# Kernel optimization log

Measured on AMD Instinct MI355X. Metric: run time of the kernel, lower is better.

The kernel has to match this reference:

```python
import jax, jax.numpy as jnp
import numpy as np

N = 50000      # nodes
E = 800000     # edges (avg degree 16)
NF, EF, H, OUT, K = 16, 8, 64, 8, 3
N_MID = 2      # n_gnn_layers=4 -> first + 2 mid + last


def setup_inputs() -> dict:
    key = jax.random.key(0)
    ks = jax.random.split(key, 16)
    s = 0.05
    return {
        "x": jax.random.normal(ks[0], (N, NF), dtype=jnp.float32),
        "edge_index": jax.random.randint(ks[1], (2, E), 0, N, dtype=jnp.int64),
        "edge_attr": jax.random.normal(ks[2], (E, EF), dtype=jnp.float32),
        # edge_aggr MLP: Linear(EF,H) -> ReLU -> Linear(H,1)
        "mlp_W1": jax.random.normal(ks[3], (EF, H), dtype=jnp.float32) * s,
        "mlp_b1": jnp.zeros((H,), dtype=jnp.float32),
        "mlp_W2": jax.random.normal(ks[4], (H, 1), dtype=jnp.float32) * s,
        "mlp_b2": jnp.zeros((1,), dtype=jnp.float32),
        # TAGConv-style layers: K+1 linear maps each
        "W_first": jax.random.normal(ks[5], (K + 1, NF, H), dtype=jnp.float32) * s,
        "b_first": jnp.zeros((H,), dtype=jnp.float32),
        "W_mid": jax.random.normal(ks[6], (N_MID, K + 1, H, H), dtype=jnp.float32) * s,
        "b_mid": jnp.zeros((N_MID, H), dtype=jnp.float32),
        "W_last": jax.random.normal(ks[7], (K + 1, H, OUT), dtype=jnp.float32) * s,
        "b_last": jnp.zeros((OUT,), dtype=jnp.float32),
    }


def _gcn_norm(edge_weight, src, dst, n_nodes):
    # deg computed at target (col), D^{-1/2} A D^{-1/2}, no self loops
    deg = jax.ops.segment_sum(edge_weight, dst, num_segments=n_nodes)
    dinv = jnp.where(deg > 0, jax.lax.rsqrt(jnp.where(deg > 0, deg, 1.0)), 0.0)
    return dinv[src] * edge_weight * dinv[dst]  # [E]


def _tag_conv(x, Ws, b, src, dst, norm, n_nodes):
    # out = sum_k (A_norm^k x) W_k + b
    out = x @ Ws[0]
    h = x
    for k in range(1, Ws.shape[0]):
        h = jax.ops.segment_sum(h[src] * norm[:, None], dst, num_segments=n_nodes)
        out = out + h @ Ws[k]
    return out + b


def reference(x, edge_index, edge_attr, mlp_W1, mlp_b1, mlp_W2, mlp_b2,
              W_first, b_first, W_mid, b_mid, W_last, b_last):
    src, dst = edge_index[0], edge_index[1]
    n_nodes = x.shape[0]
    # edge MLP -> scalar edge weight per edge
    ew = (jax.nn.relu(edge_attr @ mlp_W1 + mlp_b1) @ mlp_W2 + mlp_b2)[:, 0]  # [E]
    norm = _gcn_norm(ew, src, dst, n_nodes)
    h = jax.nn.relu(_tag_conv(x, W_first, b_first, src, dst, norm, n_nodes))
    for i in range(W_mid.shape[0]):
        h = jax.nn.relu(_tag_conv(h, W_mid[i], b_mid[i], src, dst, norm, n_nodes))
    return _tag_conv(h, W_last, b_last, src, dst, norm, n_nodes)
```

## Files before the change

### kernel.cpp

```cpp
#include <hip/hip_runtime.h>
#include <stdint.h>

#define N_NODES 50000
#define N_EDGES 800000
#define NFEAT   16
#define EFEAT   8
#define HID     64
#define OUTF    8
#define NMID    2
#define NX      (N_NODES * NFEAT)
#define NPW     16
#define CAP     64
#define PGB     ((N_NODES + 4 * NPW - 1) / (4 * NPW))
#define PPB     ((N_NODES + 15) / 16)
#define NWB     ((N_NODES + 3) / 4)

typedef unsigned short ushort_t;
typedef unsigned int   uint_t;
typedef unsigned long long ull_t;
typedef __bf16 bf16x8 __attribute__((ext_vector_type(8)));
typedef float  f32x4  __attribute__((ext_vector_type(4)));

__device__ __forceinline__ float b2f(ushort_t u) {
    return __uint_as_float(((uint_t)u) << 16);
}
__device__ __forceinline__ ushort_t f2b(float f) {
    uint_t u = __float_as_uint(f);
    return (ushort_t)((u + 0x7fffu + ((u >> 16) & 1u)) >> 16);
}
__device__ __forceinline__ float h2f(ushort_t u) {
    union { ushort_t u; _Float16 h; } c; c.u = u; return (float)c.h;
}
__device__ __forceinline__ ushort_t f2h(float f) {
    union { ushort_t u; _Float16 h; } c; c.h = (_Float16)f; return c.u;
}

__global__ __launch_bounds__(256) void edge_mlp_kernel(
    const float* __restrict__ ea, const float* __restrict__ x,
    const int* __restrict__ ei,
    const float* __restrict__ W1, const float* __restrict__ b1,
    const float* __restrict__ W2, const float* __restrict__ b2,
    ushort_t* __restrict__ xb, float* __restrict__ ew,
    int* __restrict__ cnts, uint_t* __restrict__ bucket)
{
    int tid = threadIdx.x;
    int e = blockIdx.x * 256 + tid;
    if (e >= N_EDGES) return;

    int d = ei[N_EDGES + e];
    int pos = atomicAdd(&cnts[d], 1);
    if (pos < CAP)
        bucket[(size_t)d * CAP + pos] = (uint_t)e;

    xb[e] = f2b(x[e]);

    float4 v0 = ((const float4*)ea)[2 * e];
    float4 v1 = ((const float4*)ea)[2 * e + 1];
    float a[8] = {v0.x, v0.y, v0.z, v0.w, v1.x, v1.y, v1.z, v1.w};

    float h[HID];
    #pragma unroll
    for (int j = 0; j < HID; ++j) h[j] = b1[j];

    #pragma unroll
    for (int i = 0; i < EFEAT; ++i) {
        float ai = a[i];
        #pragma unroll
        for (int j = 0; j < HID; ++j)
            h[j] = fmaf(ai, W1[i * HID + j], h[j]);
    }

    float acc = b2[0];
    #pragma unroll
    for (int j = 0; j < HID; ++j)
        acc = fmaf(fmaxf(h[j], 0.f), W2[j], acc);

    ew[e] = acc;
}

__global__ __launch_bounds__(256) void degdinv_kernel(
    int* __restrict__ cnts, const uint_t* __restrict__ bucket,
    const float* __restrict__ ew, float* __restrict__ dinv)
{
    int tid = threadIdx.x;
    int n = blockIdx.x * 4 + (tid >> 6);
    int lane = tid & 63;
    if (n >= N_NODES) return;
    int c = cnts[n]; if (c > CAP) c = CAP;
    float w = 0.f;
    if (lane < c)
        w = ew[bucket[(size_t)n * CAP + lane]];
    #pragma unroll
    for (int o = 32; o; o >>= 1) w += __shfl_down(w, o, 64);
    if (lane == 0) {
        cnts[n] = c;
        dinv[n] = (w > 0.f) ? (1.f / sqrtf(w)) : 0.f;
    }
}

__global__ __launch_bounds__(256) void rescale_kernel(
    const int* __restrict__ cnts, const float* __restrict__ dinv,
    const float* __restrict__ ew, const int* __restrict__ ei,
    uint_t* __restrict__ bucket)
{
    int tid = threadIdx.x;
    int n = blockIdx.x * 4 + (tid >> 6);
    int lane = tid & 63;
    if (n >= N_NODES) return;
    int c = cnts[n];
    float dn = dinv[n];
    if (lane < c) {
        uint_t e = bucket[(size_t)n * CAP + lane];
        int s = ei[e];
        float nv = dinv[s] * ew[e] * dn;
        nv = fminf(fmaxf(nv, -60000.f), 60000.f);
        bucket[(size_t)n * CAP + lane] = (((uint_t)f2h(nv)) << 16) | (uint_t)s;
    }
}

template<int W>
__global__ __launch_bounds__(256, 6) void prop_kernel(
    const ushort_t* __restrict__ gsrc, ushort_t* __restrict__ gout,
    const int* __restrict__ cnts, const uint_t* __restrict__ bucket)
{
    int tid = threadIdx.x;
    int wv = tid >> 6, lane = tid & 63;
    int nb = (blockIdx.x * 4 + wv) * 4;
    if (nb >= N_NODES) return;

    int cv = (lane < 4) ? cnts[nb + lane] : 0;
    int c0 = __builtin_amdgcn_readlane(cv, 0);
    int c1 = __builtin_amdgcn_readlane(cv, 1);
    int c2 = __builtin_amdgcn_readlane(cv, 2);
    int c3 = __builtin_amdgcn_readlane(cv, 3);
    int cm = max(max(c0, c1), max(c2, c3));

    uint_t p0 = 0, p1 = 0, p2 = 0, p3 = 0;
    if (lane < c0) p0 = bucket[(size_t)(nb + 0) * CAP + lane];
    if (lane < c1) p1 = bucket[(size_t)(nb + 1) * CAP + lane];
    if (lane < c2) p2 = bucket[(size_t)(nb + 2) * CAP + lane];
    if (lane < c3) p3 = bucket[(size_t)(nb + 3) * CAP + lane];

    if (W == 64) {
        float s[4][4];
        #pragma unroll
        for (int n = 0; n < 4; ++n)
            #pragma unroll
            for (int k = 0; k < 4; ++k) s[n][k] = 0.f;

        for (int j = 0; j < cm; j += 4) {
            float hv[4][4], nv[4][4];
            #pragma unroll
            for (int k = 0; k < 4; ++k) {
                int pe0 = __builtin_amdgcn_readlane((int)p0, j + k);
                int pe1 = __builtin_amdgcn_readlane((int)p1, j + k);
                int pe2 = __builtin_amdgcn_readlane((int)p2, j + k);
                int pe3 = __builtin_amdgcn_readlane((int)p3, j + k);
                nv[0][k] = h2f((ushort_t)(((uint_t)pe0) >> 16));
                nv[1][k] = h2f((ushort_t)(((uint_t)pe1) >> 16));
                nv[2][k] = h2f((ushort_t)(((uint_t)pe2) >> 16));
                nv[3][k] = h2f((ushort_t)(((uint_t)pe3) >> 16));
                hv[0][k] = b2f(gsrc[(size_t)(pe0 & 0xffff) * 64 + lane]);
                hv[1][k] = b2f(gsrc[(size_t)(pe1 & 0xffff) * 64 + lane]);
                hv[2][k] = b2f(gsrc[(size_t)(pe2 & 0xffff) * 64 + lane]);
                hv[3][k] = b2f(gsrc[(size_t)(pe3 & 0xffff) * 64 + lane]);
            }
            #pragma unroll
            for (int n = 0; n < 4; ++n)
                #pragma unroll
                for (int k = 0; k < 4; ++k)
                    s[n][k] = fmaf(hv[n][k], nv[n][k], s[n][k]);
        }

        #pragma unroll
        for (int n = 0; n < 4; ++n) {
            float v = (s[n][0] + s[n][1]) + (s[n][2] + s[n][3]);
            gout[(size_t)(nb + n) * 64 + lane] = f2b(v);
        }
    } else {
        const int il = lane & 15;
        const int quad = lane >> 4;
        float s0 = 0.f, s1 = 0.f, s2 = 0.f, s3 = 0.f;

        #pragma unroll 2
        for (int j = 0; j < cm; j += 4) {
            int jq = j + quad;
            int w0 = __shfl((int)p0, jq, 64);
            int w1 = __shfl((int)p1, jq, 64);
            int w2 = __shfl((int)p2, jq, 64);
            int w3 = __shfl((int)p3, jq, 64);
            float h0 = b2f(gsrc[(size_t)(w0 & 0xffff) * 16 + il]);
            float h1 = b2f(gsrc[(size_t)(w1 & 0xffff) * 16 + il]);
            float h2 = b2f(gsrc[(size_t)(w2 & 0xffff) * 16 + il]);
            float h3 = b2f(gsrc[(size_t)(w3 & 0xffff) * 16 + il]);
            s0 = fmaf(h0, h2f((ushort_t)(((uint_t)w0) >> 16)), s0);
            s1 = fmaf(h1, h2f((ushort_t)(((uint_t)w1) >> 16)), s1);
            s2 = fmaf(h2, h2f((ushort_t)(((uint_t)w2) >> 16)), s2);
            s3 = fmaf(h3, h2f((ushort_t)(((uint_t)w3) >> 16)), s3);
        }

        s0 += __shfl_xor(s0, 16, 64); s0 += __shfl_xor(s0, 32, 64);
        s1 += __shfl_xor(s1, 16, 64); s1 += __shfl_xor(s1, 32, 64);
        s2 += __shfl_xor(s2, 16, 64); s2 += __shfl_xor(s2, 32, 64);
        s3 += __shfl_xor(s3, 16, 64); s3 += __shfl_xor(s3, 32, 64);
        if (lane < 16) {
            gout[(size_t)(nb + 0) * 16 + lane] = f2b(s0);
            gout[(size_t)(nb + 1) * 16 + lane] = f2b(s1);
            gout[(size_t)(nb + 2) * 16 + lane] = f2b(s2);
            gout[(size_t)(nb + 3) * 16 + lane] = f2b(s3);
        }
    }
}

template<int F32OUT>
__global__ __launch_bounds__(256, 8) void prop8_kernel(
    const ushort_t* __restrict__ gsrc, int GS, int GO,
    const ushort_t* __restrict__ add, int AS, int AO,
    ushort_t* __restrict__ outb, float* __restrict__ outf,
    const int* __restrict__ cnts, const uint_t* __restrict__ bucket)
{
    int tid = threadIdx.x;
    int wv = tid >> 6, lane = tid & 63;
    int nb = (blockIdx.x * 4 + wv) * 4;
    if (nb >= N_NODES) return;
    const int oct = lane >> 3, il = lane & 7;

    int cv = (lane < 4) ? cnts[nb + lane] : 0;
    int c0 = __builtin_amdgcn_readlane(cv, 0);
    int c1 = __builtin_amdgcn_readlane(cv, 1);
    int c2 = __builtin_amdgcn_readlane(cv, 2);
    int c3 = __builtin_amdgcn_readlane(cv, 3);
    int cm = max(max(c0, c1), max(c2, c3));

    uint_t p0 = 0, p1 = 0, p2 = 0, p3 = 0;
    if (lane < c0) p0 = bucket[(size_t)(nb + 0) * CAP + lane];
    if (lane < c1) p1 = bucket[(size_t)(nb + 1) * CAP + lane];
    if (lane < c2) p2 = bucket[(size_t)(nb + 2) * CAP + lane];
    if (lane < c3) p3 = bucket[(size_t)(nb + 3) * CAP + lane];

    float s0 = 0.f, s1 = 0.f, s2 = 0.f, s3 = 0.f;

    #pragma unroll 2
    for (int j = 0; j < cm; j += 8) {
        int jo = j + oct;
        int w0 = __shfl((int)p0, jo, 64);
        int w1 = __shfl((int)p1, jo, 64);
        int w2 = __shfl((int)p2, jo, 64);
        int w3 = __shfl((int)p3, jo, 64);
        float h0 = b2f(gsrc[(size_t)(w0 & 0xffff) * GS + GO + il]);
        float h1 = b2f(gsrc[(size_t)(w1 & 0xffff) * GS + GO + il]);
        float h2 = b2f(gsrc[(size_t)(w2 & 0xffff) * GS + GO + il]);
        float h3 = b2f(gsrc[(size_t)(w3 & 0xffff) * GS + GO + il]);
        s0 = fmaf(h0, h2f((ushort_t)(((uint_t)w0) >> 16)), s0);
        s1 = fmaf(h1, h2f((ushort_t)(((uint_t)w1) >> 16)), s1);
        s2 = fmaf(h2, h2f((ushort_t)(((uint_t)w2) >> 16)), s2);
        s3 = fmaf(h3, h2f((ushort_t)(((uint_t)w3) >> 16)), s3);
    }

    #define FIN(sN, n)                                                               \
        {                                                                            \
            float s = sN;                                                            \
            s += __shfl_xor(s, 8, 64);                                               \
            s += __shfl_xor(s, 16, 64);                                              \
            s += __shfl_xor(s, 32, 64);                                              \
            if (lane < 8) {                                                          \
                float v = s + b2f(add[(size_t)(nb + n) * AS + AO + lane]);           \
                if (F32OUT) outf[(size_t)(nb + n) * 8 + lane] = v;                   \
                else        outb[(size_t)(nb + n) * 8 + lane] = f2b(v);              \
            }                                                                        \
        }
    FIN(s0, 0)
    FIN(s1, 1)
    FIN(s2, 2)
    FIN(s3, 3)
    #undef FIN
}

template<int SRCW, int COUT, int ACT>
__global__ __launch_bounds__(256, 4) void gemm4_kernel(
    const ushort_t* __restrict__ s0, const ushort_t* __restrict__ s1,
    const ushort_t* __restrict__ s2, const ushort_t* __restrict__ s3,
    const float* __restrict__ Wg,
    const float* __restrict__ bias,
    ushort_t* __restrict__ outb)
{
    constexpr int NCH = (SRCW == 16) ? 2 : 8;
    constexpr int NT  = (COUT + 15) / 16;
    __shared__ __align__(16) ushort_t Bp[NCH * NT * 512];

    int tid = threadIdx.x;
    for (int idx = tid; idx < NCH * NT * 512; idx += 256) {
        int f = idx >> 9;
        int l = (idx >> 3) & 63, j = idx & 7;
        int ch = f / NT, nt = f - ch * NT;
        int kk = ((l >> 4) << 3) + j;
        int n = nt * 16 + (l & 15);
        int widx, krow;
        if (SRCW == 16) { widx = 2 * ch + (kk >> 4); krow = kk & 15; }
        else            { widx = ch >> 1;            krow = ((ch & 1) << 5) + kk; }
        float v = (n < COUT) ? Wg[((size_t)widx * SRCW + krow) * COUT + n] : 0.f;
        Bp[idx] = f2b(v);
    }
    __syncthreads();

    int wv = tid >> 6, lane = tid & 63;
    int node_base = (blockIdx.x * 4 + wv) * NPW;
    if (node_base >= N_NODES) return;
    int m = lane & 15, quad = lane >> 4;

    const ushort_t* srcs[4] = {s0, s1, s2, s3};
    bf16x8 a[NCH];
    #pragma unroll
    for (int ch = 0; ch < NCH; ++ch) {
        const ushort_t* sp;
        size_t off;
        if (SRCW == 16) {
            sp = (quad < 2) ? srcs[2 * ch] : srcs[2 * ch + 1];
            off = (size_t)(node_base + m) * 16 + (quad & 1) * 8;
        } else {
            sp = srcs[ch >> 1];
            off = (size_t)(node_base + m) * 64 + ((ch & 1) << 5) + quad * 8;
        }
        a[ch] = *(const bf16x8*)(sp + off);
    }

    #pragma unroll
    for (int nt = 0; nt < NT; ++nt) {
        float bv = bias[(nt * 16 + m) & (COUT - 1)];
        f32x4 c = {bv, bv, bv, bv};
        #pragma unroll
        for (int ch = 0; ch < NCH; ++ch) {
            bf16x8 b = *(const bf16x8*)&Bp[((ch * NT + nt) * 64 + lane) * 8];
            c = __builtin_amdgcn_mfma_f32_16x16x32_bf16(a[ch], b, c, 0, 0, 0);
        }
        #pragma unroll
        for (int r = 0; r < 4; ++r) {
            int row = node_base + quad * 4 + r;
            float v = ACT ? fmaxf(c[r], 0.f) : c[r];
            outb[(size_t)row * COUT + nt * 16 + m] = f2b(v);
        }
    }
}

__global__ __launch_bounds__(256, 4) void gemmL_kernel(
    const ushort_t* __restrict__ src,
    const float* __restrict__ Wl,
    const float* __restrict__ bl,
    ushort_t* __restrict__ Z)
{
    __shared__ __align__(16) ushort_t Bp[2 * 2 * 512];

    int tid = threadIdx.x;
    for (int idx = tid; idx < 2048; idx += 256) {
        int f = idx >> 9;
        int ch = f >> 1, nt = f & 1;
        int l = (idx >> 3) & 63, j = idx & 7;
        int kg = ch * 32 + ((l >> 4) << 3) + j;
        int n = nt * 16 + (l & 15);
        int widx = n >> 3, col = n & 7;
        Bp[idx] = f2b(Wl[((size_t)widx * 64 + kg) * 8 + col]);
    }
    __syncthreads();

    int wv = tid >> 6, lane = tid & 63;
    int node_base = (blockIdx.x * 4 + wv) * NPW;
    if (node_base >= N_NODES) return;
    int m = lane & 15, quad = lane >> 4;

    bf16x8 a[2];
    #pragma unroll
    for (int ch = 0; ch < 2; ++ch)
        a[ch] = *(const bf16x8*)(src + (size_t)(node_base + m) * 64 + ch * 32 + quad * 8);

    #pragma unroll
    for (int nt = 0; nt < 2; ++nt) {
        int n = nt * 16 + m;
        float bv = (n < 8) ? bl[n] : 0.f;
        f32x4 c = {bv, bv, bv, bv};
        #pragma unroll
        for (int ch = 0; ch < 2; ++ch) {
            bf16x8 b = *(const bf16x8*)&Bp[((ch * 2 + nt) * 64 + lane) * 8];
            c = __builtin_amdgcn_mfma_f32_16x16x32_bf16(a[ch], b, c, 0, 0, 0);
        }
        #pragma unroll
        for (int r = 0; r < 4; ++r) {
            int row = node_base + quad * 4 + r;
            Z[(size_t)row * 32 + n] = f2b(c[r]);
        }
    }
}

extern "C" void kernel_launch(void* const* d_in, const int* in_sizes, int n_in,
                              void* d_out, int out_size, void* d_ws, size_t ws_size,
                              hipStream_t stream)
{
    const float* x  = (const float*)d_in[0];
    const int*   ei = (const int*)d_in[1];
    const float* ea = (const float*)d_in[2];
    const float* W1 = (const float*)d_in[3];
    const float* b1 = (const float*)d_in[4];
    const float* W2 = (const float*)d_in[5];
    const float* b2 = (const float*)d_in[6];
    const float* Wf = (const float*)d_in[7];
    const float* bf = (const float*)d_in[8];
    const float* Wm = (const float*)d_in[9];
    const float* bm = (const float*)d_in[10];
    const float* Wl = (const float*)d_in[11];
    const float* bl = (const float*)d_in[12];

    char* ws = (char*)d_ws;
    size_t off = 0;
    auto take = [&](size_t bytes) -> char* {
        char* p = ws + off;
        off = (off + bytes + 255) & ~(size_t)255;
        return p;
    };
    int*      cnts   = (int*)take((size_t)N_NODES * 4);
    float*    dinv   = (float*)take((size_t)N_NODES * 4);
    float*    ew     = (float*)take((size_t)N_EDGES * 4);
    uint_t*   bucket = (uint_t*)take((size_t)N_NODES * CAP * 4);
    ushort_t* xb     = (ushort_t*)take((size_t)NX * 2 + 256);
    ushort_t* g1     = (ushort_t*)take((size_t)N_NODES * HID * 2 + 256);
    ushort_t* g2     = (ushort_t*)take((size_t)N_NODES * HID * 2 + 256);
    ushort_t* g3     = (ushort_t*)take((size_t)N_NODES * HID * 2 + 256);
    ushort_t* curA   = (ushort_t*)take((size_t)N_NODES * HID * 2 + 256);
    ushort_t* curB   = (ushort_t*)take((size_t)N_NODES * HID * 2 + 256);
    ushort_t* Z      = (ushort_t*)take((size_t)N_NODES * 32 * 2 + 256);
    ushort_t* t8a    = (ushort_t*)take((size_t)N_NODES * 8 * 2 + 256);
    ushort_t* t8b    = (ushort_t*)take((size_t)N_NODES * 8 * 2 + 256);

    hipMemsetAsync(cnts, 0, (size_t)N_NODES * 4, stream);

    const int EB = (N_EDGES + 255) / 256;

    edge_mlp_kernel<<<EB, 256, 0, stream>>>(ea, x, ei, W1, b1, W2, b2, xb, ew, cnts, bucket);
    degdinv_kernel<<<NWB, 256, 0, stream>>>(cnts, bucket, ew, dinv);
    rescale_kernel<<<NWB, 256, 0, stream>>>(cnts, dinv, ew, ei, bucket);

    prop_kernel<NFEAT><<<PPB, 256, 0, stream>>>(xb, g1, cnts, bucket);
    prop_kernel<NFEAT><<<PPB, 256, 0, stream>>>(g1, g2, cnts, bucket);
    prop_kernel<NFEAT><<<PPB, 256, 0, stream>>>(g2, g3, cnts, bucket);
    gemm4_kernel<NFEAT, HID, 1><<<PGB, 256, 0, stream>>>(
        xb, g1, g2, g3, Wf, bf, curA);

    ushort_t* cin = curA;
    ushort_t* cot = curB;
    for (int L = 0; L < NMID; ++L) {
        prop_kernel<HID><<<PPB, 256, 0, stream>>>(cin, g1, cnts, bucket);
        prop_kernel<HID><<<PPB, 256, 0, stream>>>(g1, g2, cnts, bucket);
        prop_kernel<HID><<<PPB, 256, 0, stream>>>(g2, g3, cnts, bucket);
        gemm4_kernel<HID, HID, 1><<<PGB, 256, 0, stream>>>(
            cin, g1, g2, g3, Wm + (size_t)L * 4 * HID * HID, bm + L * HID, cot);
        ushort_t* t = cin; cin = cot; cot = t;
    }

    gemmL_kernel<<<PGB, 256, 0, stream>>>(cin, Wl, bl, Z);
    prop8_kernel<0><<<PPB, 256, 0, stream>>>(Z, 32, 24, Z, 32, 16, t8a, nullptr, cnts, bucket);
    prop8_kernel<0><<<PPB, 256, 0, stream>>>(t8a, 8, 0, Z, 32, 8, t8b, nullptr, cnts, bucket);
    prop8_kernel<1><<<PPB, 256, 0, stream>>>(t8b, 8, 0, Z, 32, 0, nullptr, (float*)d_out, cnts, bucket);
}
```

Baseline: 413.4 us.

## Pack edge weight and source into 64-bit buckets and double-buffer HID gather loads

The edge MLP kernel now writes the raw edge weight and source index together into a 64-bit per-destination bucket. This removes the separate ew array and the indirect ew[e] and ei[e] gathers in the degree and rescale kernels, and rescale writes the packed half-weight/source entries into a separate 32-bit bucket. Separately, the 64-wide propagation loop is software-pipelined with two register buffers so the next group of neighbor loads is issued before the current FMAs. The cost is a larger bucket workspace and higher register pressure in prop_kernel<64>.

```diff
diff --git a/kernel.cpp b/kernel.cpp
--- a/kernel.cpp
+++ b/kernel.cpp
@@ -40,8 +40,8 @@
     const int* __restrict__ ei,
     const float* __restrict__ W1, const float* __restrict__ b1,
     const float* __restrict__ W2, const float* __restrict__ b2,
-    ushort_t* __restrict__ xb, float* __restrict__ ew,
-    int* __restrict__ cnts, uint_t* __restrict__ bucket)
+    ushort_t* __restrict__ xb,
+    int* __restrict__ cnts, ull_t* __restrict__ bucket8)
 {
     int tid = threadIdx.x;
     int e = blockIdx.x * 256 + tid;
@@ -49,8 +49,7 @@
 
     int d = ei[N_EDGES + e];
     int pos = atomicAdd(&cnts[d], 1);
-    if (pos < CAP)
-        bucket[(size_t)d * CAP + pos] = (uint_t)e;
+    int sn = ei[e];
 
     xb[e] = f2b(x[e]);
 
@@ -75,12 +74,14 @@
     for (int j = 0; j < HID; ++j)
         acc = fmaf(fmaxf(h[j], 0.f), W2[j], acc);
 
-    ew[e] = acc;
+    if (pos < CAP)
+        bucket8[(size_t)d * CAP + pos] =
+            (((ull_t)__float_as_uint(acc)) << 32) | (uint_t)sn;
 }
 
 __global__ __launch_bounds__(256) void degdinv_kernel(
-    int* __restrict__ cnts, const uint_t* __restrict__ bucket,
-    const float* __restrict__ ew, float* __restrict__ dinv)
+    int* __restrict__ cnts, const ull_t* __restrict__ bucket8,
+    float* __restrict__ dinv)
 {
     int tid = threadIdx.x;
     int n = blockIdx.x * 4 + (tid >> 6);
@@ -89,7 +90,7 @@
     int c = cnts[n]; if (c > CAP) c = CAP;
     float w = 0.f;
     if (lane < c)
-        w = ew[bucket[(size_t)n * CAP + lane]];
+        w = __uint_as_float((uint_t)(bucket8[(size_t)n * CAP + lane] >> 32));
     #pragma unroll
     for (int o = 32; o; o >>= 1) w += __shfl_down(w, o, 64);
     if (lane == 0) {
@@ -100,8 +101,7 @@
 
 __global__ __launch_bounds__(256) void rescale_kernel(
     const int* __restrict__ cnts, const float* __restrict__ dinv,
-    const float* __restrict__ ew, const int* __restrict__ ei,
-    uint_t* __restrict__ bucket)
+    const ull_t* __restrict__ bucket8, uint_t* __restrict__ bucket4)
 {
     int tid = threadIdx.x;
     int n = blockIdx.x * 4 + (tid >> 6);
@@ -110,11 +110,12 @@
     int c = cnts[n];
     float dn = dinv[n];
     if (lane < c) {
-        uint_t e = bucket[(size_t)n * CAP + lane];
-        int s = ei[e];
-        float nv = dinv[s] * ew[e] * dn;
+        ull_t q = bucket8[(size_t)n * CAP + lane];
+        uint_t s = (uint_t)q;
+        float ewv = __uint_as_float((uint_t)(q >> 32));
+        float nv = dinv[s] * ewv * dn;
         nv = fminf(fmaxf(nv, -60000.f), 60000.f);
-        bucket[(size_t)n * CAP + lane] = (((uint_t)f2h(nv)) << 16) | (uint_t)s;
+        bucket4[(size_t)n * CAP + lane] = (((uint_t)f2h(nv)) << 16) | s;
     }
 }
 
@@ -148,29 +149,43 @@
             #pragma unroll
             for (int k = 0; k < 4; ++k) s[n][k] = 0.f;
 
-        for (int j = 0; j < cm; j += 4) {
-            float hv[4][4], nv[4][4];
-            #pragma unroll
-            for (int k = 0; k < 4; ++k) {
-                int pe0 = __builtin_amdgcn_readlane((int)p0, j + k);
-                int pe1 = __builtin_amdgcn_readlane((int)p1, j + k);
-                int pe2 = __builtin_amdgcn_readlane((int)p2, j + k);
-                int pe3 = __builtin_amdgcn_readlane((int)p3, j + k);
-                nv[0][k] = h2f((ushort_t)(((uint_t)pe0) >> 16));
-                nv[1][k] = h2f((ushort_t)(((uint_t)pe1) >> 16));
-                nv[2][k] = h2f((ushort_t)(((uint_t)pe2) >> 16));
-                nv[3][k] = h2f((ushort_t)(((uint_t)pe3) >> 16));
-                hv[0][k] = b2f(gsrc[(size_t)(pe0 & 0xffff) * 64 + lane]);
-                hv[1][k] = b2f(gsrc[(size_t)(pe1 & 0xffff) * 64 + lane]);
-                hv[2][k] = b2f(gsrc[(size_t)(pe2 & 0xffff) * 64 + lane]);
-                hv[3][k] = b2f(gsrc[(size_t)(pe3 & 0xffff) * 64 + lane]);
+        float hvA[16], hvB[16];
+        int   peA[16], peB[16];
+
+        #define LOADQ(HV, PE, J)                                                     \
+            { _Pragma("unroll")                                                      \
+              for (int k = 0; k < 4; ++k) {                                          \
+                  PE[0*4+k] = __builtin_amdgcn_readlane((int)p0, (J) + k);           \
+                  PE[1*4+k] = __builtin_amdgcn_readlane((int)p1, (J) + k);           \
+                  PE[2*4+k] = __builtin_amdgcn_readlane((int)p2, (J) + k);           \
+                  PE[3*4+k] = __builtin_amdgcn_readlane((int)p3, (J) + k);           \
+                  HV[0*4+k] = b2f(gsrc[(size_t)(PE[0*4+k] & 0xffff) * 64 + lane]);   \
+                  HV[1*4+k] = b2f(gsrc[(size_t)(PE[1*4+k] & 0xffff) * 64 + lane]);   \
+                  HV[2*4+k] = b2f(gsrc[(size_t)(PE[2*4+k] & 0xffff) * 64 + lane]);   \
+                  HV[3*4+k] = b2f(gsrc[(size_t)(PE[3*4+k] & 0xffff) * 64 + lane]);   \
+              } }
+
+        #define FMAQ(HV, PE)                                                         \
+            { _Pragma("unroll")                                                      \
+              for (int n = 0; n < 4; ++n)                                            \
+                  _Pragma("unroll")                                                  \
+                  for (int k = 0; k < 4; ++k)                                        \
+                      s[n][k] = fmaf(HV[n*4+k],                                      \
+                          h2f((ushort_t)(((uint_t)PE[n*4+k]) >> 16)), s[n][k]); }
+
+        int nsteps = (cm + 3) >> 2;
+        if (nsteps > 0) {
+            LOADQ(hvA, peA, 0)
+            for (int t = 1; t < nsteps; t += 2) {
+                LOADQ(hvB, peB, t * 4)
+                FMAQ(hvA, peA)
+                if (t + 1 < nsteps) LOADQ(hvA, peA, (t + 1) * 4)
+                FMAQ(hvB, peB)
             }
-            #pragma unroll
-            for (int n = 0; n < 4; ++n)
-                #pragma unroll
-                for (int k = 0; k < 4; ++k)
-                    s[n][k] = fmaf(hv[n][k], nv[n][k], s[n][k]);
-        }
+            if (nsteps & 1) FMAQ(hvA, peA)
+        }
+        #undef LOADQ
+        #undef FMAQ
 
         #pragma unroll
         for (int n = 0; n < 4; ++n) {
@@ -415,47 +430,47 @@
         off = (off + bytes + 255) & ~(size_t)255;
         return p;
     };
-    int*      cnts   = (int*)take((size_t)N_NODES * 4);
-    float*    dinv   = (float*)take((size_t)N_NODES * 4);
-    float*    ew     = (float*)take((size_t)N_EDGES * 4);
-    uint_t*   bucket = (uint_t*)take((size_t)N_NODES * CAP * 4);
-    ushort_t* xb     = (ushort_t*)take((size_t)NX * 2 + 256);
-    ushort_t* g1     = (ushort_t*)take((size_t)N_NODES * HID * 2 + 256);
-    ushort_t* g2     = (ushort_t*)take((size_t)N_NODES * HID * 2 + 256);
-    ushort_t* g3     = (ushort_t*)take((size_t)N_NODES * HID * 2 + 256);
-    ushort_t* curA   = (ushort_t*)take((size_t)N_NODES * HID * 2 + 256);
-    ushort_t* curB   = (ushort_t*)take((size_t)N_NODES * HID * 2 + 256);
-    ushort_t* Z      = (ushort_t*)take((size_t)N_NODES * 32 * 2 + 256);
-    ushort_t* t8a    = (ushort_t*)take((size_t)N_NODES * 8 * 2 + 256);
-    ushort_t* t8b    = (ushort_t*)take((size_t)N_NODES * 8 * 2 + 256);
+    int*      cnts    = (int*)take((size_t)N_NODES * 4);
+    float*    dinv    = (float*)take((size_t)N_NODES * 4);
+    ull_t*    bucket8 = (ull_t*)take((size_t)N_NODES * CAP * 8);
+    uint_t*   bucket4 = (uint_t*)take((size_t)N_NODES * CAP * 4);
+    ushort_t* xb      = (ushort_t*)take((size_t)NX * 2 + 256);
+    ushort_t* g1      = (ushort_t*)take((size_t)N_NODES * HID * 2 + 256);
+    ushort_t* g2      = (ushort_t*)take((size_t)N_NODES * HID * 2 + 256);
+    ushort_t* g3      = (ushort_t*)take((size_t)N_NODES * HID * 2 + 256);
+    ushort_t* curA    = (ushort_t*)take((size_t)N_NODES * HID * 2 + 256);
+    ushort_t* curB    = (ushort_t*)take((size_t)N_NODES * HID * 2 + 256);
+    ushort_t* Z       = (ushort_t*)take((size_t)N_NODES * 32 * 2 + 256);
+    ushort_t* t8a     = (ushort_t*)take((size_t)N_NODES * 8 * 2 + 256);
+    ushort_t* t8b     = (ushort_t*)take((size_t)N_NODES * 8 * 2 + 256);
 
     hipMemsetAsync(cnts, 0, (size_t)N_NODES * 4, stream);
 
     const int EB = (N_EDGES + 255) / 256;
 
-    edge_mlp_kernel<<<EB, 256, 0, stream>>>(ea, x, ei, W1, b1, W2, b2, xb, ew, cnts, bucket);
-    degdinv_kernel<<<NWB, 256, 0, stream>>>(cnts, bucket, ew, dinv);
-    rescale_kernel<<<NWB, 256, 0, stream>>>(cnts, dinv, ew, ei, bucket);
-
-    prop_kernel<NFEAT><<<PPB, 256, 0, stream>>>(xb, g1, cnts, bucket);
-    prop_kernel<NFEAT><<<PPB, 256, 0, stream>>>(g1, g2, cnts, bucket);
-    prop_kernel<NFEAT><<<PPB, 256, 0, stream>>>(g2, g3, cnts, bucket);
+    edge_mlp_kernel<<<EB, 256, 0, stream>>>(ea, x, ei, W1, b1, W2, b2, xb, cnts, bucket8);
+    degdinv_kernel<<<NWB, 256, 0, stream>>>(cnts, bucket8, dinv);
+    rescale_kernel<<<NWB, 256, 0, stream>>>(cnts, dinv, bucket8, bucket4);
+
+    prop_kernel<NFEAT><<<PPB, 256, 0, stream>>>(xb, g1, cnts, bucket4);
+    prop_kernel<NFEAT><<<PPB, 256, 0, stream>>>(g1, g2, cnts, bucket4);
+    prop_kernel<NFEAT><<<PPB, 256, 0, stream>>>(g2, g3, cnts, bucket4);
     gemm4_kernel<NFEAT, HID, 1><<<PGB, 256, 0, stream>>>(
         xb, g1, g2, g3, Wf, bf, curA);
 
     ushort_t* cin = curA;
     ushort_t* cot = curB;
     for (int L = 0; L < NMID; ++L) {
-        prop_kernel<HID><<<PPB, 256, 0, stream>>>(cin, g1, cnts, bucket);
-        prop_kernel<HID><<<PPB, 256, 0, stream>>>(g1, g2, cnts, bucket);
-        prop_kernel<HID><<<PPB, 256, 0, stream>>>(g2, g3, cnts, bucket);
+        prop_kernel<HID><<<PPB, 256, 0, stream>>>(cin, g1, cnts, bucket4);
+        prop_kernel<HID><<<PPB, 256, 0, stream>>>(g1, g2, cnts, bucket4);
+        prop_kernel<HID><<<PPB, 256, 0, stream>>>(g2, g3, cnts, bucket4);
         gemm4_kernel<HID, HID, 1><<<PGB, 256, 0, stream>>>(
             cin, g1, g2, g3, Wm + (size_t)L * 4 * HID * HID, bm + L * HID, cot);
         ushort_t* t = cin; cin = cot; cot = t;
     }
 
     gemmL_kernel<<<PGB, 256, 0, stream>>>(cin, Wl, bl, Z);
-    prop8_kernel<0><<<PPB, 256, 0, stream>>>(Z, 32, 24, Z, 32, 16, t8a, nullptr, cnts, bucket);
-    prop8_kernel<0><<<PPB, 256, 0, stream>>>(t8a, 8, 0, Z, 32, 8, t8b, nullptr, cnts, bucket);
-    prop8_kernel<1><<<PPB, 256, 0, stream>>>(t8b, 8, 0, Z, 32, 0, nullptr, (float*)d_out, cnts, bucket);
-}
+    prop8_kernel<0><<<PPB, 256, 0, stream>>>(Z, 32, 24, Z, 32, 16, t8a, nullptr, cnts, bucket4);
+    prop8_kernel<0><<<PPB, 256, 0, stream>>>(t8a, 8, 0, Z, 32, 8, t8b, nullptr, cnts, bucket4);
+    prop8_kernel<1><<<PPB, 256, 0, stream>>>(t8b, 8, 0, Z, 32, 0, nullptr, (float*)d_out, cnts, bucket4);
+}
```

Measured after the change: 485.0 us. 1.17x slower.
